# Kernel tuning notes

Measured on AMD Instinct MI355X. Metric: run time of the kernel, lower is better.

The kernel has to match this reference:

```python
import jax, jax.numpy as jnp
import numpy as np

TAU = 0.5
EPS = 1e-8


def setup_inputs() -> dict:
    key = jax.random.key(0)
    k1, k2 = jax.random.split(key)
    N, D = 200000, 512
    z_pos = jax.random.normal(k1, (N, D), dtype=jnp.float32)
    W = jax.random.normal(k2, (D, D), dtype=jnp.float32) * (1.0 / np.sqrt(D))
    b = jnp.zeros((D,), dtype=jnp.float32)
    return {"z_pos": z_pos, "W": W, "b": b}


def reference(z_pos, W, b):
    # sample_centroid: softmax-weighted centroid (computed on detached embeddings)
    h = jax.lax.stop_gradient(z_pos)
    init_c = h.mean(axis=0)                              # [D]
    d2 = jnp.sum((h - init_c[None, :]) ** 2, axis=1)     # [N]
    w = jax.nn.softmax(-d2 / TAU)                        # [N]
    c = jnp.sum(h * w[:, None], axis=0)                  # [D]

    # SimNet: dist = 1 - cosine_similarity(proj(x), c)
    x_proj = z_pos @ W.T + b                             # [N, D]
    x_norm = jnp.maximum(jnp.linalg.norm(x_proj, axis=-1), EPS)  # [N]
    c_norm = jnp.maximum(jnp.linalg.norm(c), EPS)
    cos = (x_proj @ c) / (x_norm * c_norm)               # [N]
    dist = 1.0 - cos
    return dist
```

## Files before the change

### kernel.cpp

```cpp
#include <hip/hip_runtime.h>
#include <hip/hip_bf16.h>
#include <math.h>

#define DD 512
#define EPSF 1e-8f
#define BM 128
#define BN 128
#define BK 32
#define FBIG 3.402823466e+38f
#define NPART 2048

typedef __bf16 bf16_t;
typedef __bf16 bf16x4_t __attribute__((ext_vector_type(4)));
typedef __bf16 bf16x8_t __attribute__((ext_vector_type(8)));
typedef float f32x4 __attribute__((ext_vector_type(4)));

__global__ void k_convW(const float* __restrict__ W, bf16_t* __restrict__ Wb) {
    int i = blockIdx.x * blockDim.x + threadIdx.x;
    float4 v = ((const float4*)W)[i];
    bf16x4_t o;
    o[0] = (bf16_t)v.x; o[1] = (bf16_t)v.y; o[2] = (bf16_t)v.z; o[3] = (bf16_t)v.w;
    ((bf16x4_t*)Wb)[i] = o;
}

template<bool CONV>
__global__ void k_colsum(const float* __restrict__ z, bf16_t* __restrict__ zb,
                         float* __restrict__ part, int N, int rpb) {
    int t = threadIdx.x;
    int b = blockIdx.x;
    int col4 = t & 127, sub = t >> 7;
    int r0 = b * rpb, r1 = min(r0 + rpb, N);
    const float4* z4 = (const float4*)z;
    float4 acc = make_float4(0.f, 0.f, 0.f, 0.f);
    #pragma unroll 4
    for (int r = r0 + sub; r < r1; r += 2) {
        float4 v = z4[(size_t)r * 128 + col4];
        if (CONV) {
            bf16x4_t o;
            o[0] = (bf16_t)v.x; o[1] = (bf16_t)v.y; o[2] = (bf16_t)v.z; o[3] = (bf16_t)v.w;
            ((bf16x4_t*)zb)[(size_t)r * 128 + col4] = o;
        }
        acc.x += v.x; acc.y += v.y; acc.z += v.z; acc.w += v.w;
    }
    __shared__ float4 sm[128];
    if (sub == 1) sm[col4] = acc;
    __syncthreads();
    if (sub == 0) {
        float4 o = sm[col4];
        acc.x += o.x; acc.y += o.y; acc.z += o.z; acc.w += o.w;
        ((float4*)(part + (size_t)b * DD))[col4] = acc;
    }
}

__global__ void k_reduceP(const float* __restrict__ part, float* __restrict__ outv, float scale) {
    __shared__ float sm[256];
    int j = blockIdx.x;
    int t = threadIdx.x;
    float s = 0.f;
    #pragma unroll
    for (int p = 0; p < NPART / 256; ++p) s += part[(size_t)(p * 256 + t) * DD + j];
    sm[t] = s;
    __syncthreads();
    for (int st = 128; st > 0; st >>= 1) {
        if (t < st) sm[t] += sm[t + st];
        __syncthreads();
    }
    if (t == 0) outv[j] = sm[0] * scale;
}

__global__ __launch_bounds__(256, 4) void k_d2w(
    const float* __restrict__ z, const float* __restrict__ cbar,
    float* __restrict__ part, float* __restrict__ mpart,
    float* __restrict__ spart, int N)
{
    __shared__ float4 cs[128];
    __shared__ float4 vsm[4][128];
    __shared__ float wm[4], wsv[4];
    int t = threadIdx.x;
    int lane = t & 63, wv = t >> 6;
    int l15 = lane & 15, r4 = lane >> 4;
    if (t < 128) cs[t] = ((const float4*)cbar)[t];
    __syncthreads();

    int gw = (blockIdx.x * 256 + t) >> 6;
    int nw = (gridDim.x * 256) >> 6;
    float m = FBIG, s = 0.f;
    float4 acc[8];
    #pragma unroll
    for (int q = 0; q < 8; ++q) acc[q] = make_float4(0.f, 0.f, 0.f, 0.f);

    for (int r = gw * 4 + r4; r < N; r += nw * 4) {
        const float4* zr = (const float4*)(z + (size_t)r * DD);
        float4 vv[8];
        float sum = 0.f;
        #pragma unroll
        for (int q = 0; q < 8; ++q) {
            float4 v = zr[q * 16 + l15];
            float4 c = cs[q * 16 + l15];
            vv[q] = v;
            float d;
            d = v.x - c.x; sum += d * d;
            d = v.y - c.y; sum += d * d;
            d = v.z - c.z; sum += d * d;
            d = v.w - c.w; sum += d * d;
        }
        #pragma unroll
        for (int off = 1; off < 16; off <<= 1) sum += __shfl_xor(sum, off, 64);
        float w;
        if (sum < m) {
            float f = __expf(-2.0f * (m - sum));
            s *= f;
            #pragma unroll
            for (int q = 0; q < 8; ++q) {
                acc[q].x *= f; acc[q].y *= f; acc[q].z *= f; acc[q].w *= f;
            }
            m = sum;
            w = 1.0f;
        } else {
            w = __expf(-2.0f * (sum - m));
        }
        s += w;
        #pragma unroll
        for (int q = 0; q < 8; ++q) {
            acc[q].x += w * vv[q].x; acc[q].y += w * vv[q].y;
            acc[q].z += w * vv[q].z; acc[q].w += w * vv[q].w;
        }
    }

    float mw = fminf(m, __shfl_xor(m, 16, 64));
    mw = fminf(mw, __shfl_xor(mw, 32, 64));
    float f = __expf(-2.0f * (m - mw));
    s *= f;
    #pragma unroll
    for (int q = 0; q < 8; ++q) {
        acc[q].x *= f; acc[q].y *= f; acc[q].z *= f; acc[q].w *= f;
    }
    #pragma unroll
    for (int off = 16; off < 64; off <<= 1) {
        s += __shfl_xor(s, off, 64);
        #pragma unroll
        for (int q = 0; q < 8; ++q) {
            acc[q].x += __shfl_xor(acc[q].x, off, 64);
            acc[q].y += __shfl_xor(acc[q].y, off, 64);
            acc[q].z += __shfl_xor(acc[q].z, off, 64);
            acc[q].w += __shfl_xor(acc[q].w, off, 64);
        }
    }
    if (lane < 16) {
        #pragma unroll
        for (int q = 0; q < 8; ++q) vsm[wv][q * 16 + l15] = acc[q];
        if (lane == 0) { wm[wv] = mw; wsv[wv] = s; }
    }
    __syncthreads();
    if (t < 128) {
        float M = fminf(fminf(wm[0], wm[1]), fminf(wm[2], wm[3]));
        float4 o = make_float4(0.f, 0.f, 0.f, 0.f);
        #pragma unroll
        for (int w2 = 0; w2 < 4; ++w2) {
            float fw = __expf(-2.0f * (wm[w2] - M));
            float4 a = vsm[w2][t];
            o.x += fw * a.x; o.y += fw * a.y; o.z += fw * a.z; o.w += fw * a.w;
        }
        ((float4*)(part + (size_t)blockIdx.x * DD))[t] = o;
        if (t == 0) {
            float S = 0.f;
            #pragma unroll
            for (int w2 = 0; w2 < 4; ++w2) S += wsv[w2] * __expf(-2.0f * (wm[w2] - M));
            mpart[blockIdx.x] = M;
            spart[blockIdx.x] = S;
        }
    }
}

__global__ void k_combine2(const float* __restrict__ mpart, const float* __restrict__ spart,
                           float* __restrict__ wscale) {
    __shared__ float smm[256], sms[256];
    int t = threadIdx.x;
    float M = FBIG;
    for (int i = t; i < NPART; i += 256) M = fminf(M, mpart[i]);
    smm[t] = M;
    __syncthreads();
    for (int st = 128; st > 0; st >>= 1) {
        if (t < st) smm[t] = fminf(smm[t], smm[t + st]);
        __syncthreads();
    }
    M = smm[0];
    float S = 0.f;
    for (int i = t; i < NPART; i += 256) S += spart[i] * __expf(-2.0f * (mpart[i] - M));
    sms[t] = S;
    __syncthreads();
    for (int st = 128; st > 0; st >>= 1) {
        if (t < st) sms[t] += sms[t + st];
        __syncthreads();
    }
    float inv = 1.0f / sms[0];
    for (int i = t; i < NPART; i += 256) wscale[i] = __expf(-2.0f * (mpart[i] - M)) * inv;
}

__global__ void k_reducePW(const float* __restrict__ part, const float* __restrict__ wscale,
                           float* __restrict__ outv) {
    __shared__ float sm[256];
    int j = blockIdx.x, t = threadIdx.x;
    float s = 0.f;
    #pragma unroll
    for (int p = 0; p < NPART / 256; ++p) {
        int b = p * 256 + t;
        s += part[(size_t)b * DD + j] * wscale[b];
    }
    sm[t] = s;
    __syncthreads();
    for (int st = 128; st > 0; st >>= 1) {
        if (t < st) sm[t] += sm[t + st];
        __syncthreads();
    }
    if (t == 0) outv[j] = sm[0];
}

__global__ void k_cnorm(const float* __restrict__ cvec, float* __restrict__ outp) {
    __shared__ float sm[512];
    float v = cvec[threadIdx.x];
    sm[threadIdx.x] = v * v;
    __syncthreads();
    for (int st = 256; st > 0; st >>= 1) {
        if (threadIdx.x < st) sm[threadIdx.x] += sm[threadIdx.x + st];
        __syncthreads();
    }
    if (threadIdx.x == 0) outp[0] = 1.0f / fmaxf(sqrtf(sm[0]), EPSF);
}

template<bool ZB>
__global__ __launch_bounds__(256, 4) void k_gemm(
    const float* __restrict__ z, const bf16_t* __restrict__ zb,
    const bf16_t* __restrict__ Wb, const float* __restrict__ bvec,
    const float* __restrict__ cvec, float* __restrict__ sqp, float* __restrict__ dtp,
    int N, int npad)
{
    __shared__ bf16_t As[BM * BK];
    __shared__ bf16_t Bs[BN * BK];
    __shared__ float psq[BM][8];
    __shared__ float pdt[BM][8];

    const int t    = threadIdx.x;
    const int lane = t & 63;
    const int wv   = t >> 6;
    const int wr   = wv >> 1;
    const int wc   = wv & 1;
    const int quad = lane >> 4;
    const int l15  = lane & 15;
    const int cb   = blockIdx.x;
    const int row0 = blockIdx.y * BM;

    const bf16_t* bp = Wb + (size_t)(cb * BN + (t >> 2)) * DD + (t & 3) * 8;
    const bf16_t* ap = zb + (size_t)(row0 + (t >> 2)) * DD + (t & 3) * 8;

    const int arow = t >> 1;
    const int ah   = t & 1;
    int rowe = row0 + arow; if (rowe >= N) rowe = N - 1;
    const float4* zp4 = (const float4*)(z + (size_t)rowe * DD + ah * 16);

    f32x4 acc[4][4];
    #pragma unroll
    for (int a = 0; a < 4; ++a)
        #pragma unroll
        for (int b = 0; b < 4; ++b) acc[a][b] = (f32x4){0.f, 0.f, 0.f, 0.f};

    float4 v0, v1, v2, v3;
    if (!ZB) { v0 = zp4[0]; v1 = zp4[1]; v2 = zp4[2]; v3 = zp4[3]; }

    for (int kc = 0; kc < DD; kc += BK) {
        if (kc) __syncthreads();

        #pragma unroll
        for (int q = 0; q < 2; ++q) {
            int ldsoff = __builtin_amdgcn_readfirstlane(q * 4096 + wv * 1024);
            __builtin_amdgcn_global_load_lds(
                (const __attribute__((address_space(1))) unsigned int*)(const void*)(bp + (size_t)q * 64 * DD + kc),
                (__attribute__((address_space(3))) unsigned int*)(void*)((char*)Bs + ldsoff),
                16, 0, 0);
        }
        if (ZB) {
            #pragma unroll
            for (int q = 0; q < 2; ++q) {
                int ldsoff = __builtin_amdgcn_readfirstlane(q * 4096 + wv * 1024);
                __builtin_amdgcn_global_load_lds(
                    (const __attribute__((address_space(1))) unsigned int*)(const void*)(ap + (size_t)q * 64 * DD + kc),
                    (__attribute__((address_space(3))) unsigned int*)(void*)((char*)As + ldsoff),
                    16, 0, 0);
            }
        } else {
            bf16x8_t lo, hi;
            lo[0]=(bf16_t)v0.x; lo[1]=(bf16_t)v0.y; lo[2]=(bf16_t)v0.z; lo[3]=(bf16_t)v0.w;
            lo[4]=(bf16_t)v1.x; lo[5]=(bf16_t)v1.y; lo[6]=(bf16_t)v1.z; lo[7]=(bf16_t)v1.w;
            hi[0]=(bf16_t)v2.x; hi[1]=(bf16_t)v2.y; hi[2]=(bf16_t)v2.z; hi[3]=(bf16_t)v2.w;
            hi[4]=(bf16_t)v3.x; hi[5]=(bf16_t)v3.y; hi[6]=(bf16_t)v3.z; hi[7]=(bf16_t)v3.w;
            *(bf16x8_t*)(As + arow * BK + ah * 16)     = lo;
            *(bf16x8_t*)(As + arow * BK + ah * 16 + 8) = hi;
        }

        __syncthreads();

        if (!ZB && kc + BK < DD) {
            int kf = (kc + BK) >> 2;
            v0 = zp4[kf]; v1 = zp4[kf + 1]; v2 = zp4[kf + 2]; v3 = zp4[kf + 3];
        }

        bf16x8_t af[4];
        #pragma unroll
        for (int rt = 0; rt < 4; ++rt)
            af[rt] = *(const bf16x8_t*)(As + (wr * 64 + rt * 16 + l15) * BK + quad * 8);
        #pragma unroll
        for (int ct = 0; ct < 4; ++ct) {
            bf16x8_t bfv = *(const bf16x8_t*)(Bs + (wc * 64 + ct * 16 + l15) * BK + quad * 8);
            #pragma unroll
            for (int rt = 0; rt < 4; ++rt)
                acc[rt][ct] = __builtin_amdgcn_mfma_f32_16x16x32_bf16(af[rt], bfv, acc[rt][ct], 0, 0, 0);
        }
    }

    float bc[4], cc[4];
    #pragma unroll
    for (int ct = 0; ct < 4; ++ct) {
        int col = cb * BN + wc * 64 + ct * 16 + l15;
        bc[ct] = bvec[col];
        cc[ct] = cvec[col];
    }
    #pragma unroll
    for (int rt = 0; rt < 4; ++rt) {
        #pragma unroll
        for (int rg = 0; rg < 4; ++rg) {
            float sq = 0.f, dt = 0.f;
            #pragma unroll
            for (int ct = 0; ct < 4; ++ct) {
                float x = acc[rt][ct][rg] + bc[ct];
                sq += x * x;
                dt += x * cc[ct];
            }
            sq += __shfl_xor(sq, 1, 64); dt += __shfl_xor(dt, 1, 64);
            sq += __shfl_xor(sq, 2, 64); dt += __shfl_xor(dt, 2, 64);
            if ((l15 & 3) == 0) {
                int rl = wr * 64 + rt * 16 + quad * 4 + rg;
                psq[rl][wc * 4 + (l15 >> 2)] = sq;
                pdt[rl][wc * 4 + (l15 >> 2)] = dt;
            }
        }
    }
    __syncthreads();
    if (t < BM) {
        int r = row0 + t;
        if (r < N) {
            float sq = 0.f, dt = 0.f;
            #pragma unroll
            for (int i = 0; i < 8; ++i) { sq += psq[t][i]; dt += pdt[t][i]; }
            sqp[(size_t)cb * npad + r] = sq;
            dtp[(size_t)cb * npad + r] = dt;
        }
    }
}

__global__ void k_final(const float* __restrict__ sqp, const float* __restrict__ dtp,
                        const float* __restrict__ cninv, float* __restrict__ out,
                        int N, int npad) {
    int r = blockIdx.x * blockDim.x + threadIdx.x;
    if (r < N) {
        float sq = sqp[r] + sqp[(size_t)npad + r] + sqp[2 * (size_t)npad + r] + sqp[3 * (size_t)npad + r];
        float dt = dtp[r] + dtp[(size_t)npad + r] + dtp[2 * (size_t)npad + r] + dtp[3 * (size_t)npad + r];
        out[r] = 1.0f - dt * cninv[0] / fmaxf(sqrtf(sq), EPSF);
    }
}

extern "C" void kernel_launch(void* const* d_in, const int* in_sizes, int n_in,
                              void* d_out, int out_size, void* d_ws, size_t ws_size,
                              hipStream_t stream)
{
    const float* z = (const float*)d_in[0];
    const float* W = (const float*)d_in[1];
    const float* b = (const float*)d_in[2];
    float* out = (float*)d_out;
    int N = in_sizes[0] / DD;
    int npad = ((N + BM - 1) / BM) * BM;

    float* ws = (float*)d_ws;
    size_t off = 0;
    float* part   = ws + off; off += (size_t)NPART * DD;
    float* cbar   = ws + off; off += DD;
    float* mpart  = ws + off; off += NPART;
    float* spart  = ws + off; off += NPART;
    float* wscale = ws + off; off += NPART;
    float* cvec   = ws + off; off += DD;
    float* cninv  = ws + off; off += 1;
    off = (off + 3) & ~(size_t)3;
    float* sqp    = ws + off; off += (size_t)4 * npad;
    float* dtp    = ws + off; off += (size_t)4 * npad;
    bf16_t* Wb    = (bf16_t*)(ws + off); off += (size_t)DD * DD / 2;
    bf16_t* zb    = (bf16_t*)(ws + off);
    size_t need_bytes = (off + (size_t)npad * DD / 2) * sizeof(float);
    const bool use_zb = ws_size >= need_bytes;

    int rpb = (N + NPART - 1) / NPART;

    k_convW<<<256, 256, 0, stream>>>(W, Wb);
    if (use_zb) k_colsum<true ><<<NPART, 256, 0, stream>>>(z, zb, part, N, rpb);
    else        k_colsum<false><<<NPART, 256, 0, stream>>>(z, zb, part, N, rpb);
    k_reduceP<<<DD, 256, 0, stream>>>(part, cbar, 1.0f / (float)N);
    k_d2w<<<NPART, 256, 0, stream>>>(z, cbar, part, mpart, spart, N);
    k_combine2<<<1, 256, 0, stream>>>(mpart, spart, wscale);
    k_reducePW<<<DD, 256, 0, stream>>>(part, wscale, cvec);
    k_cnorm<<<1, DD, 0, stream>>>(cvec, cninv);
    dim3 grid(4, npad / BM);
    if (use_zb) k_gemm<true ><<<grid, 256, 0, stream>>>(z, zb, Wb, b, cvec, sqp, dtp, N, npad);
    else        k_gemm<false><<<grid, 256, 0, stream>>>(z, zb, Wb, b, cvec, sqp, dtp, N, npad);
    k_final<<<(N + 255) / 256, 256, 0, stream>>>(sqp, dtp, cninv, out, N, npad);
}
```

Before: 878.8 us.

## Replace GEMM with 256x256 tile, double-buffered, swizzled LDS kernel

```diff
diff --git a/kernel.cpp b/kernel.cpp
--- a/kernel.cpp
+++ b/kernel.cpp
@@ -14,6 +14,10 @@
 typedef __bf16 bf16x4_t __attribute__((ext_vector_type(4)));
 typedef __bf16 bf16x8_t __attribute__((ext_vector_type(8)));
 typedef float f32x4 __attribute__((ext_vector_type(4)));
+
+__device__ inline float bf2f(unsigned short u) {
+    return __uint_as_float(((unsigned int)u) << 16);
+}
 
 __global__ void k_convW(const float* __restrict__ W, bf16_t* __restrict__ Wb) {
     int i = blockIdx.x * blockDim.x + threadIdx.x;
@@ -228,31 +232,178 @@
     if (threadIdx.x == 0) outp[0] = 1.0f / fmaxf(sqrtf(sm[0]), EPSF);
 }
 
-template<bool ZB>
-__global__ __launch_bounds__(256, 4) void k_gemm(
-    const float* __restrict__ z, const bf16_t* __restrict__ zb,
-    const bf16_t* __restrict__ Wb, const float* __restrict__ bvec,
-    const float* __restrict__ cvec, float* __restrict__ sqp, float* __restrict__ dtp,
-    int N, int npad)
+__global__ __launch_bounds__(512, 2) void k_gemm256(
+    const bf16_t* __restrict__ zb, const bf16_t* __restrict__ Wb,
+    const float* __restrict__ bvec, const float* __restrict__ cvec,
+    float* __restrict__ sqp, float* __restrict__ dtp, int N, int npad)
 {
-    __shared__ bf16_t As[BM * BK];
-    __shared__ bf16_t Bs[BN * BK];
+    __shared__ bf16_t As[2 * 256 * 64];
+    __shared__ bf16_t Bs[2 * 256 * 64];
+
+    const int t    = threadIdx.x;
+    const int lane = t & 63;
+    const int wid  = t >> 6;
+    const int wr   = wid >> 2;
+    const int wc   = wid & 3;
+    const int quad = lane >> 4;
+    const int l15  = lane & 15;
+
+    const int nwg = gridDim.x * gridDim.y;
+    const int lid = blockIdx.y * gridDim.x + blockIdx.x;
+    const int q8  = nwg >> 3, r8 = nwg & 7;
+    const int xcd = lid & 7, idx = lid >> 3;
+    const int wg  = (xcd < r8 ? xcd * (q8 + 1) : r8 * (q8 + 1) + (xcd - r8) * q8) + idx;
+    const int cb     = wg & 1;
+    const int row0   = (wg >> 1) * 256;
+
+    const int tr = t >> 3;
+    const int bo = ((t & 7) * 16) ^ ((tr & 7) << 4);
+    const char* apt = (const char*)zb + (size_t)(row0 + tr) * (DD * 2) + bo;
+    const char* bpt = (const char*)Wb + (size_t)(cb * 256 + tr) * (DD * 2) + bo;
+    const int ldsw = __builtin_amdgcn_readfirstlane(wid * 1024);
+
+#define STAGE256(buf, kt) do {                                                              \
+    _Pragma("unroll")                                                                       \
+    for (int r_ = 0; r_ < 4; ++r_) {                                                        \
+        __builtin_amdgcn_global_load_lds(                                                   \
+            (const __attribute__((address_space(1))) unsigned int*)(const void*)            \
+                (apt + (size_t)r_ * 65536 + (kt) * 128),                                    \
+            (__attribute__((address_space(3))) unsigned int*)(void*)                        \
+                ((char*)As + (buf) * 32768 + r_ * 8192 + ldsw), 16, 0, 0);                  \
+        __builtin_amdgcn_global_load_lds(                                                   \
+            (const __attribute__((address_space(1))) unsigned int*)(const void*)            \
+                (bpt + (size_t)r_ * 65536 + (kt) * 128),                                    \
+            (__attribute__((address_space(3))) unsigned int*)(void*)                        \
+                ((char*)Bs + (buf) * 32768 + r_ * 8192 + ldsw), 16, 0, 0);                  \
+    }                                                                                       \
+} while (0)
+
+    const int ka0 = (quad * 16) ^ ((l15 & 7) << 4);
+    const int ka1 = ka0 ^ 64;
+    const char* abase = (const char*)As + (wr * 128 + l15) * 128;
+    const char* bbase = (const char*)Bs + (wc * 64 + l15) * 128;
+
+    f32x4 acc[8][4];
+    #pragma unroll
+    for (int m = 0; m < 8; ++m)
+        #pragma unroll
+        for (int n = 0; n < 4; ++n) acc[m][n] = (f32x4){0.f, 0.f, 0.f, 0.f};
+
+    STAGE256(0, 0);
+    STAGE256(1, 1);
+    asm volatile("s_waitcnt vmcnt(8)" ::: "memory");
+    __builtin_amdgcn_sched_barrier(0);
+    __builtin_amdgcn_s_barrier();
+    __builtin_amdgcn_sched_barrier(0);
+
+    #pragma unroll
+    for (int kt = 0; kt < 8; ++kt) {
+        const int cur = kt & 1;
+        bf16x8_t afr[8][2], bfr[4][2];
+        #pragma unroll
+        for (int m = 0; m < 8; ++m) {
+            afr[m][0] = *(const bf16x8_t*)(abase + cur * 32768 + m * 2048 + ka0);
+            afr[m][1] = *(const bf16x8_t*)(abase + cur * 32768 + m * 2048 + ka1);
+        }
+        #pragma unroll
+        for (int n = 0; n < 4; ++n) {
+            bfr[n][0] = *(const bf16x8_t*)(bbase + cur * 32768 + n * 2048 + ka0);
+            bfr[n][1] = *(const bf16x8_t*)(bbase + cur * 32768 + n * 2048 + ka1);
+        }
+        asm volatile("s_waitcnt lgkmcnt(0)" ::: "memory");
+        __builtin_amdgcn_sched_barrier(0);
+        __builtin_amdgcn_s_barrier();
+        __builtin_amdgcn_sched_barrier(0);
+        if (kt < 6) STAGE256(cur, kt + 2);
+        __builtin_amdgcn_sched_barrier(0);
+        __builtin_amdgcn_s_setprio(1);
+        #pragma unroll
+        for (int s = 0; s < 2; ++s)
+            #pragma unroll
+            for (int m = 0; m < 8; ++m)
+                #pragma unroll
+                for (int n = 0; n < 4; ++n)
+                    acc[m][n] = __builtin_amdgcn_mfma_f32_16x16x32_bf16(
+                        afr[m][s], bfr[n][s], acc[m][n], 0, 0, 0);
+        __builtin_amdgcn_s_setprio(0);
+        if (kt < 6) { asm volatile("s_waitcnt vmcnt(8)" ::: "memory"); }
+        else        { asm volatile("s_waitcnt vmcnt(0)" ::: "memory"); }
+        __builtin_amdgcn_sched_barrier(0);
+        __builtin_amdgcn_s_barrier();
+        __builtin_amdgcn_sched_barrier(0);
+    }
+#undef STAGE256
+
+    float* psq = (float*)As;
+    float* pdt = (float*)((char*)As + 16384);
+    float bc[4], cc[4];
+    #pragma unroll
+    for (int n = 0; n < 4; ++n) {
+        int col = cb * 256 + wc * 64 + n * 16 + l15;
+        bc[n] = bvec[col];
+        cc[n] = cvec[col];
+    }
+    #pragma unroll
+    for (int m = 0; m < 8; ++m) {
+        #pragma unroll
+        for (int rg = 0; rg < 4; ++rg) {
+            float sq = 0.f, dt = 0.f;
+            #pragma unroll
+            for (int n = 0; n < 4; ++n) {
+                float x = acc[m][n][rg] + bc[n];
+                sq += x * x;
+                dt += x * cc[n];
+            }
+            sq += __shfl_xor(sq, 1, 64); dt += __shfl_xor(dt, 1, 64);
+            sq += __shfl_xor(sq, 2, 64); dt += __shfl_xor(dt, 2, 64);
+            if ((l15 & 3) == 0) {
+                int row = wr * 128 + m * 16 + quad * 4 + rg;
+                int slot = wc * 4 + (l15 >> 2);
+                psq[row * 16 + slot] = sq;
+                pdt[row * 16 + slot] = dt;
+            }
+        }
+    }
+    __syncthreads();
+    if (t < 256) {
+        int r = row0 + t;
+        if (r < N) {
+            const float4* p4 = (const float4*)(psq + t * 16);
+            const float4* d4 = (const float4*)(pdt + t * 16);
+            float sq = 0.f, dt = 0.f;
+            #pragma unroll
+            for (int i = 0; i < 4; ++i) {
+                float4 a = p4[i], b2 = d4[i];
+                sq += a.x + a.y + a.z + a.w;
+                dt += b2.x + b2.y + b2.z + b2.w;
+            }
+            sqp[(size_t)cb * npad + r] = sq;
+            dtp[(size_t)cb * npad + r] = dt;
+        }
+    }
+}
+
+__global__ __launch_bounds__(256, 4) void k_gemm_fb(
+    const float* __restrict__ z, const bf16_t* __restrict__ Wb,
+    const float* __restrict__ bvec, const float* __restrict__ cvec,
+    float* __restrict__ sqp, float* __restrict__ dtp, int N, int npad)
+{
+    __shared__ bf16_t Asl[BM * BK];
+    __shared__ bf16_t Bsl[BN * BK];
     __shared__ float psq[BM][8];
     __shared__ float pdt[BM][8];
 
     const int t    = threadIdx.x;
     const int lane = t & 63;
     const int wv   = t >> 6;
-    const int wr   = wv >> 1;
-    const int wc   = wv & 1;
+    const int wrr  = wv >> 1;
+    const int wcc  = wv & 1;
     const int quad = lane >> 4;
     const int l15  = lane & 15;
-    const int cb   = blockIdx.x;
+    const int cbx  = blockIdx.x;
     const int row0 = blockIdx.y * BM;
 
-    const bf16_t* bp = Wb + (size_t)(cb * BN + (t >> 2)) * DD + (t & 3) * 8;
-    const bf16_t* ap = zb + (size_t)(row0 + (t >> 2)) * DD + (t & 3) * 8;
-
+    const bf16_t* bp = Wb + (size_t)(cbx * BN + (t >> 2)) * DD + (t & 3) * 8;
     const int arow = t >> 1;
     const int ah   = t & 1;
     int rowe = row0 + arow; if (rowe >= N) rowe = N - 1;
@@ -264,53 +415,37 @@
         #pragma unroll
         for (int b = 0; b < 4; ++b) acc[a][b] = (f32x4){0.f, 0.f, 0.f, 0.f};
 
-    float4 v0, v1, v2, v3;
-    if (!ZB) { v0 = zp4[0]; v1 = zp4[1]; v2 = zp4[2]; v3 = zp4[3]; }
+    float4 v0 = zp4[0], v1 = zp4[1], v2 = zp4[2], v3 = zp4[3];
 
     for (int kc = 0; kc < DD; kc += BK) {
         if (kc) __syncthreads();
-
         #pragma unroll
         for (int q = 0; q < 2; ++q) {
             int ldsoff = __builtin_amdgcn_readfirstlane(q * 4096 + wv * 1024);
             __builtin_amdgcn_global_load_lds(
                 (const __attribute__((address_space(1))) unsigned int*)(const void*)(bp + (size_t)q * 64 * DD + kc),
-                (__attribute__((address_space(3))) unsigned int*)(void*)((char*)Bs + ldsoff),
+                (__attribute__((address_space(3))) unsigned int*)(void*)((char*)Bsl + ldsoff),
                 16, 0, 0);
         }
-        if (ZB) {
-            #pragma unroll
-            for (int q = 0; q < 2; ++q) {
-                int ldsoff = __builtin_amdgcn_readfirstlane(q * 4096 + wv * 1024);
-                __builtin_amdgcn_global_load_lds(
-                    (const __attribute__((address_space(1))) unsigned int*)(const void*)(ap + (size_t)q * 64 * DD + kc),
-                    (__attribute__((address_space(3))) unsigned int*)(void*)((char*)As + ldsoff),
-                    16, 0, 0);
-            }
-        } else {
-            bf16x8_t lo, hi;
-            lo[0]=(bf16_t)v0.x; lo[1]=(bf16_t)v0.y; lo[2]=(bf16_t)v0.z; lo[3]=(bf16_t)v0.w;
-            lo[4]=(bf16_t)v1.x; lo[5]=(bf16_t)v1.y; lo[6]=(bf16_t)v1.z; lo[7]=(bf16_t)v1.w;
-            hi[0]=(bf16_t)v2.x; hi[1]=(bf16_t)v2.y; hi[2]=(bf16_t)v2.z; hi[3]=(bf16_t)v2.w;
-            hi[4]=(bf16_t)v3.x; hi[5]=(bf16_t)v3.y; hi[6]=(bf16_t)v3.z; hi[7]=(bf16_t)v3.w;
-            *(bf16x8_t*)(As + arow * BK + ah * 16)     = lo;
-            *(bf16x8_t*)(As + arow * BK + ah * 16 + 8) = hi;
-        }
-
+        bf16x8_t lo, hi;
+        lo[0]=(bf16_t)v0.x; lo[1]=(bf16_t)v0.y; lo[2]=(bf16_t)v0.z; lo[3]=(bf16_t)v0.w;
+        lo[4]=(bf16_t)v1.x; lo[5]=(bf16_t)v1.y; lo[6]=(bf16_t)v1.z; lo[7]=(bf16_t)v1.w;
+        hi[0]=(bf16_t)v2.x; hi[1]=(bf16_t)v2.y; hi[2]=(bf16_t)v2.z; hi[3]=(bf16_t)v2.w;
+        hi[4]=(bf16_t)v3.x; hi[5]=(bf16_t)v3.y; hi[6]=(bf16_t)v3.z; hi[7]=(bf16_t)v3.w;
+        *(bf16x8_t*)(Asl + arow * BK + ah * 16)     = lo;
+        *(bf16x8_t*)(Asl + arow * BK + ah * 16 + 8) = hi;
         __syncthreads();
-
-        if (!ZB && kc + BK < DD) {
+        if (kc + BK < DD) {
             int kf = (kc + BK) >> 2;
             v0 = zp4[kf]; v1 = zp4[kf + 1]; v2 = zp4[kf + 2]; v3 = zp4[kf + 3];
         }
-
         bf16x8_t af[4];
         #pragma unroll
         for (int rt = 0; rt < 4; ++rt)
-            af[rt] = *(const bf16x8_t*)(As + (wr * 64 + rt * 16 + l15) * BK + quad * 8);
+            af[rt] = *(const bf16x8_t*)(Asl + (wrr * 64 + rt * 16 + l15) * BK + quad * 8);
         #pragma unroll
         for (int ct = 0; ct < 4; ++ct) {
-            bf16x8_t bfv = *(const bf16x8_t*)(Bs + (wc * 64 + ct * 16 + l15) * BK + quad * 8);
+            bf16x8_t bfv = *(const bf16x8_t*)(Bsl + (wcc * 64 + ct * 16 + l15) * BK + quad * 8);
             #pragma unroll
             for (int rt = 0; rt < 4; ++rt)
                 acc[rt][ct] = __builtin_amdgcn_mfma_f32_16x16x32_bf16(af[rt], bfv, acc[rt][ct], 0, 0, 0);
@@ -320,7 +455,7 @@
     float bc[4], cc[4];
     #pragma unroll
     for (int ct = 0; ct < 4; ++ct) {
-        int col = cb * BN + wc * 64 + ct * 16 + l15;
+        int col = cbx * BN + wcc * 64 + ct * 16 + l15;
         bc[ct] = bvec[col];
         cc[ct] = cvec[col];
     }
@@ -338,9 +473,9 @@
             sq += __shfl_xor(sq, 1, 64); dt += __shfl_xor(dt, 1, 64);
             sq += __shfl_xor(sq, 2, 64); dt += __shfl_xor(dt, 2, 64);
             if ((l15 & 3) == 0) {
-                int rl = wr * 64 + rt * 16 + quad * 4 + rg;
-                psq[rl][wc * 4 + (l15 >> 2)] = sq;
-                pdt[rl][wc * 4 + (l15 >> 2)] = dt;
+                int rl = wrr * 64 + rt * 16 + quad * 4 + rg;
+                psq[rl][wcc * 4 + (l15 >> 2)] = sq;
+                pdt[rl][wcc * 4 + (l15 >> 2)] = dt;
             }
         }
     }
@@ -351,19 +486,24 @@
             float sq = 0.f, dt = 0.f;
             #pragma unroll
             for (int i = 0; i < 8; ++i) { sq += psq[t][i]; dt += pdt[t][i]; }
-            sqp[(size_t)cb * npad + r] = sq;
-            dtp[(size_t)cb * npad + r] = dt;
-        }
-    }
-}
-
+            sqp[(size_t)cbx * npad + r] = sq;
+            dtp[(size_t)cbx * npad + r] = dt;
+        }
+    }
+}
+
+template<int NCB>
 __global__ void k_final(const float* __restrict__ sqp, const float* __restrict__ dtp,
                         const float* __restrict__ cninv, float* __restrict__ out,
                         int N, int npad) {
     int r = blockIdx.x * blockDim.x + threadIdx.x;
     if (r < N) {
-        float sq = sqp[r] + sqp[(size_t)npad + r] + sqp[2 * (size_t)npad + r] + sqp[3 * (size_t)npad + r];
-        float dt = dtp[r] + dtp[(size_t)npad + r] + dtp[2 * (size_t)npad + r] + dtp[3 * (size_t)npad + r];
+        float sq = 0.f, dt = 0.f;
+        #pragma unroll
+        for (int i = 0; i < NCB; ++i) {
+            sq += sqp[(size_t)i * npad + r];
+            dt += dtp[(size_t)i * npad + r];
+        }
         out[r] = 1.0f - dt * cninv[0] / fmaxf(sqrtf(sq), EPSF);
     }
 }
@@ -377,7 +517,7 @@
     const float* b = (const float*)d_in[2];
     float* out = (float*)d_out;
     int N = in_sizes[0] / DD;
-    int npad = ((N + BM - 1) / BM) * BM;
+    int npad = ((N + 255) / 256) * 256;
 
     float* ws = (float*)d_ws;
     size_t off = 0;
@@ -406,8 +546,13 @@
     k_combine2<<<1, 256, 0, stream>>>(mpart, spart, wscale);
     k_reducePW<<<DD, 256, 0, stream>>>(part, wscale, cvec);
     k_cnorm<<<1, DD, 0, stream>>>(cvec, cninv);
-    dim3 grid(4, npad / BM);
-    if (use_zb) k_gemm<true ><<<grid, 256, 0, stream>>>(z, zb, Wb, b, cvec, sqp, dtp, N, npad);
-    else        k_gemm<false><<<grid, 256, 0, stream>>>(z, zb, Wb, b, cvec, sqp, dtp, N, npad);
-    k_final<<<(N + 255) / 256, 256, 0, stream>>>(sqp, dtp, cninv, out, N, npad);
-}
+    if (use_zb) {
+        dim3 grid(2, npad / 256);
+        k_gemm256<<<grid, 512, 0, stream>>>(zb, Wb, b, cvec, sqp, dtp, N, npad);
+        k_final<2><<<(N + 255) / 256, 256, 0, stream>>>(sqp, dtp, cninv, out, N, npad);
+    } else {
+        dim3 grid(4, npad / BM);
+        k_gemm_fb<<<grid, 256, 0, stream>>>(z, Wb, b, cvec, sqp, dtp, N, npad);
+        k_final<4><<<(N + 255) / 256, 256, 0, stream>>>(sqp, dtp, cninv, out, N, npad);
+    }
+}
```

Measured after the change: 857.5 us. 1.02x faster.
